# Optimization experiments

Hardware: AMD Instinct MI355X
Metric: run time of the kernel (lower is better)

Reference implementation:

```python
import jax, jax.numpy as jnp
import numpy as np

N_NODES = 100000
N_EDGES = 1600000
D_IN = 512
D_HID = 128
N_CLASSES = 100


def _gcn_norm(edge_index, n_nodes):
    # Add self loops and compute symmetric normalization D^{-1/2} (A+I) D^{-1/2}
    sl = jnp.arange(n_nodes, dtype=edge_index.dtype)
    src = jnp.concatenate([edge_index[0], sl])
    dst = jnp.concatenate([edge_index[1], sl])
    deg = jax.ops.segment_sum(jnp.ones_like(dst, dtype=jnp.float32), dst,
                              num_segments=n_nodes)
    dinv = jnp.where(deg > 0, jax.lax.rsqrt(deg), 0.0)
    norm = dinv[src] * dinv[dst]  # [E + N]
    return src, dst, norm


def _gcn_layer(x, W, b, src, dst, norm, n_nodes):
    h = x @ W                                  # [N, d_out] (transform first, like PyG GCNConv)
    msg = h[src] * norm[:, None]               # [E+N, d_out] gather + scale
    out = jax.ops.segment_sum(msg, dst, num_segments=n_nodes)  # scatter-add
    return out + b


def setup_inputs() -> dict:
    key = jax.random.key(0)
    ks = jax.random.split(key, 6)
    x = jax.random.normal(ks[0], (N_NODES, D_IN), dtype=jnp.float32)
    edge_index = jax.random.randint(ks[1], (2, N_EDGES), 0, N_NODES, dtype=jnp.int64)
    W1 = jax.random.normal(ks[2], (D_IN, D_HID), dtype=jnp.float32) * (1.0 / np.sqrt(D_IN))
    b1 = jnp.zeros((D_HID,), dtype=jnp.float32)
    W2 = jax.random.normal(ks[3], (D_HID, N_CLASSES), dtype=jnp.float32) * (1.0 / np.sqrt(D_HID))
    b2 = jnp.zeros((N_CLASSES,), dtype=jnp.float32)
    return {"x": x, "edge_index": edge_index, "W1": W1, "b1": b1, "W2": W2, "b2": b2}


def reference(x, edge_index, W1, b1, W2, b2):
    n_nodes = x.shape[0]
    src, dst, norm = _gcn_norm(edge_index, n_nodes)
    h = jax.nn.relu(_gcn_layer(x, W1, b1, src, dst, norm, n_nodes))
    logits = _gcn_layer(h, W2, b2, src, dst, norm, n_nodes)
    return jax.nn.log_softmax(logits, axis=-1)
```

## Files before the change

kernel.cpp:

```cpp
#include <hip/hip_runtime.h>
#include <math.h>

typedef __attribute__((ext_vector_type(8))) short short8;
typedef __attribute__((ext_vector_type(4))) float f32x4;
typedef _Float16 half8 __attribute__((ext_vector_type(8)));
typedef __fp16 fp16x2 __attribute__((ext_vector_type(2)));
typedef unsigned int uint;

__device__ inline uint f2bf(float f) {
    uint u = __float_as_uint(f);
    return (u + 0x7fffu + ((u >> 16) & 1u)) >> 16;
}
__device__ inline uint pack2(float lo, float hi) { return f2bf(lo) | (f2bf(hi) << 16); }
__device__ inline float bflo(uint u) { return __uint_as_float(u << 16); }
__device__ inline float bfhi(uint u) { return __uint_as_float(u & 0xffff0000u); }
__device__ inline uint cvtpk(float lo, float hi) {
    uint r;
    asm("v_cvt_pk_bf16_f32 %0, %1, %2" : "=v"(r) : "v"(lo), "v"(hi));
    return r;
}
__device__ inline uint pkh(float lo, float hi) {
    union { fp16x2 h; uint u; } c;
    c.h = __builtin_amdgcn_cvt_pkrtz(lo, hi);
    return c.u;
}

__global__ void k_degree(const int* __restrict__ dst, int E, int* __restrict__ cnt) {
    int i = blockIdx.x * 256 + threadIdx.x;
    if (i < E) atomicAdd(&cnt[dst[i]], 1);
}

__global__ void k_dinv(const int* __restrict__ cnt, float* __restrict__ dinv, int N) {
    int i = blockIdx.x * 256 + threadIdx.x;
    if (i < N) dinv[i] = rsqrtf((float)(cnt[i] + 1));
}

__global__ __launch_bounds__(512) void k_scan1(const int* __restrict__ cnt, int* __restrict__ rp,
                                               int* __restrict__ partials, int N) {
    __shared__ int s[512];
    int i = blockIdx.x * 512 + threadIdx.x;
    int v = (i < N) ? cnt[i] : 0;
    s[threadIdx.x] = v;
    __syncthreads();
    for (int d = 1; d < 512; d <<= 1) {
        int t = (threadIdx.x >= d) ? s[threadIdx.x - d] : 0;
        __syncthreads();
        s[threadIdx.x] += t;
        __syncthreads();
    }
    if (i < N) rp[i] = s[threadIdx.x] - v;
    if (threadIdx.x == 511) partials[blockIdx.x] = s[511];
}

__global__ void k_scan2(int* __restrict__ partials, int nb) {
    if (threadIdx.x == 0 && blockIdx.x == 0) {
        int acc = 0;
        for (int i = 0; i < nb; i++) { int v = partials[i]; partials[i] = acc; acc += v; }
    }
}

__global__ __launch_bounds__(512) void k_scan3(int* __restrict__ rp, const int* __restrict__ partials,
                                               int N, int E) {
    int i = blockIdx.x * 512 + threadIdx.x;
    if (i < N) rp[i] += partials[blockIdx.x];
    if (i == 0) rp[N] = E;
}

__global__ void k_fill(const int* __restrict__ src, const int* __restrict__ dst, int E,
                       const int* __restrict__ rp, int* __restrict__ cursor,
                       const float* __restrict__ dinv, float2* __restrict__ colw) {
    int i = blockIdx.x * 256 + threadIdx.x;
    if (i < E) {
        int d = dst[i];
        int s = src[i];
        int pos = rp[d] + atomicAdd(&cursor[d], 1);
        colw[pos] = make_float2(__int_as_float(s), dinv[s]);
    }
}

__global__ void k_w1prep(const float* __restrict__ W1, ushort* __restrict__ frag) {
    int tid = blockIdx.x * 256 + threadIdx.x;
    if (tid < 8192) {
        int ks = tid >> 9;
        int t = (tid >> 6) & 7;
        int l = tid & 63;
        int kbase = ks * 32 + (l >> 4) * 8;
        int c = t * 16 + (l & 15);
#pragma unroll
        for (int j = 0; j < 8; j++) {
            float v = W1[(size_t)(kbase + j) * 128 + c];
            union { _Float16 h; ushort u; } cv;
            cv.h = (_Float16)v;
            frag[(size_t)tid * 8 + j] = cv.u;
        }
    }
}

__global__ __launch_bounds__(256) void k_gemm1(const float* __restrict__ x,
                                               const uint4* __restrict__ w1f,
                                               uint* __restrict__ h1, int N) {
    __shared__ uint hsp[4][32][66];
    int tid = threadIdx.x, wv = tid >> 6, l = tid & 63;
    int cl = l & 15, kg = l >> 4;
    int n0 = blockIdx.x * 128 + wv * 32;
    int r0 = n0 + cl;       if (r0 >= N) r0 = N - 1;
    int r1 = n0 + 16 + cl;  if (r1 >= N) r1 = N - 1;
    const float* xr0 = x + (size_t)r0 * 512 + kg * 8;
    const float* xr1 = x + (size_t)r1 * 512 + kg * 8;

    f32x4 acc[2][8];
#pragma unroll
    for (int m = 0; m < 2; m++)
#pragma unroll
        for (int t = 0; t < 8; t++) acc[m][t] = (f32x4){0.f, 0.f, 0.f, 0.f};

    union U { uint4 u4; half8 h8; };

    float4 pa0[2], pa1[2];
    pa0[0] = *(const float4*)(xr0);     pa1[0] = *(const float4*)(xr0 + 4);
    pa0[1] = *(const float4*)(xr1);     pa1[1] = *(const float4*)(xr1 + 4);

    for (int ks = 0; ks < 16; ks++) {
        U A[2];
#pragma unroll
        for (int m = 0; m < 2; m++) {
            A[m].u4.x = pkh(pa0[m].x, pa0[m].y);
            A[m].u4.y = pkh(pa0[m].z, pa0[m].w);
            A[m].u4.z = pkh(pa1[m].x, pa1[m].y);
            A[m].u4.w = pkh(pa1[m].z, pa1[m].w);
        }
        uint4 bq[8];
#pragma unroll
        for (int t = 0; t < 8; t++) bq[t] = w1f[(ks * 8 + t) * 64 + l];
        if (ks < 15) {
            pa0[0] = *(const float4*)(xr0 + (ks + 1) * 32);
            pa1[0] = *(const float4*)(xr0 + (ks + 1) * 32 + 4);
            pa0[1] = *(const float4*)(xr1 + (ks + 1) * 32);
            pa1[1] = *(const float4*)(xr1 + (ks + 1) * 32 + 4);
        }
#pragma unroll
        for (int t = 0; t < 8; t++) {
            U B;
            B.u4 = bq[t];
            acc[0][t] = __builtin_amdgcn_mfma_f32_16x16x32_f16(A[0].h8, B.h8, acc[0][t], 0, 0, 0);
            acc[1][t] = __builtin_amdgcn_mfma_f32_16x16x32_f16(A[1].h8, B.h8, acc[1][t], 0, 0, 0);
        }
    }

#pragma unroll
    for (int m = 0; m < 2; m++)
#pragma unroll
        for (int t = 0; t < 8; t++)
#pragma unroll
            for (int r = 0; r < 4; r++) {
                float mine = acc[m][t][r];
                float other = __shfl_xor(mine, 1, 64);
                if ((cl & 1) == 0)
                    hsp[wv][m * 16 + kg * 4 + r][t * 8 + (cl >> 1)] = cvtpk(mine, other);
            }
#pragma unroll
    for (int it = 0; it < 32; it++) {
        int gr = n0 + it;
        if (gr < N) h1[(size_t)gr * 64 + l] = hsp[wv][it][l];
    }
}

template <bool RELU_BIAS>
__global__ __launch_bounds__(256) void k_agg(const uint* __restrict__ h, const float* __restrict__ dinv,
                                             const int* __restrict__ rp, const float2* __restrict__ colw,
                                             const float* __restrict__ bias, uint* __restrict__ outb, int N) {
    int wave = threadIdx.x >> 6, lane = threadIdx.x & 63;
    int v = blockIdx.x * 4 + wave;
    if (v >= N) return;
    float dv = dinv[v];
    float wself = dv * dv;
    uint us = h[(size_t)v * 64 + lane];
    float acc0 = bflo(us) * wself;
    float acc1 = bfhi(us) * wself;
    int e0 = rp[v], e1 = rp[v + 1];
    int i = e0;
    for (; i + 8 <= e1; i += 8) {
        float2 q[8];
        uint u[8];
#pragma unroll
        for (int j = 0; j < 8; j++) q[j] = colw[i + j];
#pragma unroll
        for (int j = 0; j < 8; j++) u[j] = h[(size_t)__float_as_int(q[j].x) * 64 + lane];
#pragma unroll
        for (int j = 0; j < 8; j++) {
            float w = q[j].y * dv;
            acc0 = fmaf(bflo(u[j]), w, acc0);
            acc1 = fmaf(bfhi(u[j]), w, acc1);
        }
    }
    if (i + 4 <= e1) {
        float2 q[4];
        uint u[4];
#pragma unroll
        for (int j = 0; j < 4; j++) q[j] = colw[i + j];
#pragma unroll
        for (int j = 0; j < 4; j++) u[j] = h[(size_t)__float_as_int(q[j].x) * 64 + lane];
#pragma unroll
        for (int j = 0; j < 4; j++) {
            float w = q[j].y * dv;
            acc0 = fmaf(bflo(u[j]), w, acc0);
            acc1 = fmaf(bfhi(u[j]), w, acc1);
        }
        i += 4;
    }
    for (; i < e1; i++) {
        float2 q = colw[i];
        uint u = h[(size_t)__float_as_int(q.x) * 64 + lane];
        float w = q.y * dv;
        acc0 = fmaf(bflo(u), w, acc0);
        acc1 = fmaf(bfhi(u), w, acc1);
    }
    if (RELU_BIAS) {
        float2 b = *(const float2*)&bias[2 * lane];
        acc0 = fmaxf(acc0 + b.x, 0.f);
        acc1 = fmaxf(acc1 + b.y, 0.f);
    }
    outb[(size_t)v * 64 + lane] = pack2(acc0, acc1);
}

__global__ void k_w2prep(const float* __restrict__ W2, const float* __restrict__ b2,
                         ushort* __restrict__ frag, float* __restrict__ b2pad) {
    int tid = blockIdx.x * 256 + threadIdx.x;
    if (tid < 1792) {
        int q = tid / 448;
        int t = (tid >> 6) % 7;
        int l = tid & 63;
        int kbase = q * 32 + (l >> 4) * 8;
        int c = t * 16 + (l & 15);
#pragma unroll
        for (int j = 0; j < 8; j++) {
            float v = (c < 100) ? W2[(kbase + j) * 100 + c] : 0.f;
            frag[(size_t)tid * 8 + j] = (ushort)f2bf(v);
        }
    } else if (tid < 1792 + 112) {
        int c = tid - 1792;
        b2pad[c] = (c < 100) ? b2[c] : -1e30f;
    }
}

__global__ __launch_bounds__(256) void k_out_mfma(const uint* __restrict__ g2u,
                                                  const uint4* __restrict__ w2fragG,
                                                  const float* __restrict__ b2pad,
                                                  float* __restrict__ out, int N) {
    __shared__ uint4 w2s[1792];
    __shared__ float b2s[112];
    int tid = threadIdx.x;
    for (int i = tid; i < 1792; i += 256) w2s[i] = w2fragG[i];
    if (tid < 112) b2s[tid] = b2pad[tid];
    __syncthreads();

    int w = tid >> 6, l = tid & 63;
    int v0 = blockIdx.x * 128 + w * 32;
    int cl = l & 15, gq = l >> 4;

    f32x4 acc[2][7];
#pragma unroll
    for (int m = 0; m < 2; m++)
#pragma unroll
        for (int t = 0; t < 7; t++) acc[m][t] = (f32x4){0.f, 0.f, 0.f, 0.f};

    union U { uint4 u4; short8 s8; };

#pragma unroll
    for (int q = 0; q < 4; q++) {
        short8 afr[2];
#pragma unroll
        for (int m = 0; m < 2; m++) {
            int rv = v0 + m * 16 + cl;
            if (rv >= N) rv = N - 1;
            U a;
            a.u4 = *(const uint4*)&g2u[(size_t)rv * 64 + q * 16 + gq * 4];
            afr[m] = a.s8;
        }
#pragma unroll
        for (int t = 0; t < 7; t++) {
            U b;
            b.u4 = w2s[(q * 7 + t) * 64 + l];
            acc[0][t] = __builtin_amdgcn_mfma_f32_16x16x32_bf16(afr[0], b.s8, acc[0][t], 0, 0, 0);
            acc[1][t] = __builtin_amdgcn_mfma_f32_16x16x32_bf16(afr[1], b.s8, acc[1][t], 0, 0, 0);
        }
    }

    float bsv[7];
#pragma unroll
    for (int t = 0; t < 7; t++) bsv[t] = b2s[t * 16 + cl];

#pragma unroll
    for (int m = 0; m < 2; m++) {
#pragma unroll
        for (int r = 0; r < 4; r++) {
            int row = v0 + m * 16 + gq * 4 + r;
            float lg[7];
#pragma unroll
            for (int t = 0; t < 7; t++) lg[t] = acc[m][t][r] + bsv[t];
            float mx = lg[0];
#pragma unroll
            for (int t = 1; t < 7; t++) mx = fmaxf(mx, lg[t]);
            mx = fmaxf(mx, __shfl_xor(mx, 1, 64));
            mx = fmaxf(mx, __shfl_xor(mx, 2, 64));
            mx = fmaxf(mx, __shfl_xor(mx, 4, 64));
            mx = fmaxf(mx, __shfl_xor(mx, 8, 64));
            float s = 0.f;
#pragma unroll
            for (int t = 0; t < 7; t++) s += __expf(lg[t] - mx);
            s += __shfl_xor(s, 1, 64);
            s += __shfl_xor(s, 2, 64);
            s += __shfl_xor(s, 4, 64);
            s += __shfl_xor(s, 8, 64);
            float lse = mx + __logf(s);
            if (row < N) {
#pragma unroll
                for (int t = 0; t < 7; t++) {
                    int c = t * 16 + cl;
                    if (c < 100) out[(size_t)row * 100 + c] = lg[t] - lse;
                }
            }
        }
    }
}

extern "C" void kernel_launch(void* const* d_in, const int* in_sizes, int n_in,
                              void* d_out, int out_size, void* d_ws, size_t ws_size,
                              hipStream_t stream) {
    const float* x  = (const float*)d_in[0];
    const int*   ei = (const int*)d_in[1];
    const float* W1 = (const float*)d_in[2];
    const float* b1 = (const float*)d_in[3];
    const float* W2 = (const float*)d_in[4];
    const float* b2 = (const float*)d_in[5];
    float* out = (float*)d_out;

    int N = in_sizes[0] / 512;
    int E = in_sizes[1] / 2;
    const int* srcI = ei;
    const int* dstI = ei + E;

    char* wsb = (char*)d_ws;
    size_t off = 0;
    auto alloc = [&](size_t bytes) {
        void* p = wsb + off;
        off = (off + bytes + 255) & ~(size_t)255;
        return p;
    };
    int*    cnt      = (int*)alloc((size_t)N * 4);
    int*    cursor   = (int*)alloc((size_t)N * 4);
    float*  dinv     = (float*)alloc((size_t)N * 4);
    int*    rp       = (int*)alloc((size_t)(N + 1) * 4);
    int*    partials = (int*)alloc(1024 * 4);
    ushort* w1f      = (ushort*)alloc(8192 * 8 * 2);
    ushort* w2frag   = (ushort*)alloc(1792 * 8 * 2);
    float*  b2pad    = (float*)alloc(112 * 4);
    float2* colw     = (float2*)alloc((size_t)E * 8);
    uint*   h1       = (uint*)alloc((size_t)N * 64 * 4);
    uint*   a1       = (uint*)alloc((size_t)N * 64 * 4);
    uint*   g2       = h1;

    hipMemsetAsync(cnt, 0, (size_t)N * 4, stream);
    hipMemsetAsync(cursor, 0, (size_t)N * 4, stream);

    k_degree<<<(E + 255) / 256, 256, 0, stream>>>(dstI, E, cnt);
    k_dinv<<<(N + 255) / 256, 256, 0, stream>>>(cnt, dinv, N);
    int nb = (N + 511) / 512;
    k_scan1<<<nb, 512, 0, stream>>>(cnt, rp, partials, N);
    k_scan2<<<1, 64, 0, stream>>>(partials, nb);
    k_scan3<<<nb, 512, 0, stream>>>(rp, partials, N, E);
    k_fill<<<(E + 255) / 256, 256, 0, stream>>>(srcI, dstI, E, rp, cursor, dinv, colw);
    k_w1prep<<<32, 256, 0, stream>>>(W1, w1f);
    k_w2prep<<<8, 256, 0, stream>>>(W2, b2, w2frag, b2pad);

    k_gemm1<<<(N + 127) / 128, 256, 0, stream>>>(x, (const uint4*)w1f, h1, N);
    k_agg<true><<<(N + 3) / 4, 256, 0, stream>>>(h1, dinv, rp, colw, b1, a1, N);
    k_agg<false><<<(N + 3) / 4, 256, 0, stream>>>(a1, dinv, rp, colw, nullptr, g2, N);
    k_out_mfma<<<(N + 127) / 128, 256, 0, stream>>>(g2, (const uint4*)w2frag, b2pad, out, N);
}
```

Before: 428.6 us.

## Stage GEMM1 x and W1 tiles through LDS with async double-buffered loads

Rewrites the first-layer GEMM so each block of 64 rows stages x and W1 fragment chunks into a 128KB double-buffered LDS region using global_load_lds, with an XOR swizzle on the x rows. Previously each wave streamed x and W1 straight from global memory into registers. The goal is to overlap the next chunk's loads with MFMA work and to share W1 across waves. In exchange, 128KB of LDS limits occupancy to one block per CU, and the tile shrinks from 128 to 64 rows per block.

```diff
diff --git a/kernel.cpp b/kernel.cpp
--- a/kernel.cpp
+++ b/kernel.cpp
@@ -23,6 +23,11 @@
     union { fp16x2 h; uint u; } c;
     c.h = __builtin_amdgcn_cvt_pkrtz(lo, hi);
     return c.u;
+}
+__device__ inline void gload16(const void* g, void* l) {
+    __builtin_amdgcn_global_load_lds(
+        (const __attribute__((address_space(1))) void*)g,
+        (__attribute__((address_space(3))) void*)l, 16, 0, 0);
 }
 
 __global__ void k_degree(const int* __restrict__ dst, int E, int* __restrict__ cnt) {
@@ -99,69 +104,75 @@
 __global__ __launch_bounds__(256) void k_gemm1(const float* __restrict__ x,
                                                const uint4* __restrict__ w1f,
                                                uint* __restrict__ h1, int N) {
-    __shared__ uint hsp[4][32][66];
+    __shared__ char lds[131072];
     int tid = threadIdx.x, wv = tid >> 6, l = tid & 63;
     int cl = l & 15, kg = l >> 4;
-    int n0 = blockIdx.x * 128 + wv * 32;
-    int r0 = n0 + cl;       if (r0 >= N) r0 = N - 1;
-    int r1 = n0 + 16 + cl;  if (r1 >= N) r1 = N - 1;
-    const float* xr0 = x + (size_t)r0 * 512 + kg * 8;
-    const float* xr1 = x + (size_t)r1 * 512 + kg * 8;
-
-    f32x4 acc[2][8];
-#pragma unroll
-    for (int m = 0; m < 2; m++)
-#pragma unroll
-        for (int t = 0; t < 8; t++) acc[m][t] = (f32x4){0.f, 0.f, 0.f, 0.f};
+    int row0 = blockIdx.x * 64;
+
+    auto stage = [&](int c) {
+        char* xbase = lds + (c & 1) * 32768;
+        char* bbase = lds + 65536 + (c & 1) * 32768;
+        const char* bsrc = (const char*)w1f + (size_t)(c * 2048) * 16;
+#pragma unroll
+        for (int i = 0; i < 8; i++) {
+            int s = wv * 512 + i * 64 + l;
+            int row = s >> 5, kk = s & 31;
+            int kslot = kk ^ (row & 7);
+            int rg = row0 + row; if (rg >= N) rg = N - 1;
+            const float* gs = x + (size_t)rg * 512 + c * 128 + kslot * 4;
+            gload16(gs, xbase + (size_t)(s - l) * 16);
+            gload16(bsrc + (size_t)s * 16, bbase + (size_t)(s - l) * 16);
+        }
+    };
+
+    f32x4 acc[8];
+#pragma unroll
+    for (int t = 0; t < 8; t++) acc[t] = (f32x4){0.f, 0.f, 0.f, 0.f};
 
     union U { uint4 u4; half8 h8; };
-
-    float4 pa0[2], pa1[2];
-    pa0[0] = *(const float4*)(xr0);     pa1[0] = *(const float4*)(xr0 + 4);
-    pa0[1] = *(const float4*)(xr1);     pa1[1] = *(const float4*)(xr1 + 4);
-
-    for (int ks = 0; ks < 16; ks++) {
-        U A[2];
-#pragma unroll
-        for (int m = 0; m < 2; m++) {
-            A[m].u4.x = pkh(pa0[m].x, pa0[m].y);
-            A[m].u4.y = pkh(pa0[m].z, pa0[m].w);
-            A[m].u4.z = pkh(pa1[m].x, pa1[m].y);
-            A[m].u4.w = pkh(pa1[m].z, pa1[m].w);
-        }
-        uint4 bq[8];
-#pragma unroll
-        for (int t = 0; t < 8; t++) bq[t] = w1f[(ks * 8 + t) * 64 + l];
-        if (ks < 15) {
-            pa0[0] = *(const float4*)(xr0 + (ks + 1) * 32);
-            pa1[0] = *(const float4*)(xr0 + (ks + 1) * 32 + 4);
-            pa0[1] = *(const float4*)(xr1 + (ks + 1) * 32);
-            pa1[1] = *(const float4*)(xr1 + (ks + 1) * 32 + 4);
-        }
-#pragma unroll
-        for (int t = 0; t < 8; t++) {
-            U B;
-            B.u4 = bq[t];
-            acc[0][t] = __builtin_amdgcn_mfma_f32_16x16x32_f16(A[0].h8, B.h8, acc[0][t], 0, 0, 0);
-            acc[1][t] = __builtin_amdgcn_mfma_f32_16x16x32_f16(A[1].h8, B.h8, acc[1][t], 0, 0, 0);
-        }
-    }
-
-#pragma unroll
-    for (int m = 0; m < 2; m++)
-#pragma unroll
-        for (int t = 0; t < 8; t++)
-#pragma unroll
-            for (int r = 0; r < 4; r++) {
-                float mine = acc[m][t][r];
-                float other = __shfl_xor(mine, 1, 64);
-                if ((cl & 1) == 0)
-                    hsp[wv][m * 16 + kg * 4 + r][t * 8 + (cl >> 1)] = cvtpk(mine, other);
+    int rowl = wv * 16 + cl;
+    int swz = cl & 7;
+
+    stage(0);
+    __syncthreads();
+    for (int c = 0; c < 4; c++) {
+        if (c < 3) stage(c + 1);
+        const char* xbase = lds + (c & 1) * 32768;
+        const char* bbase = lds + 65536 + (c & 1) * 32768;
+#pragma unroll
+        for (int ks = 0; ks < 4; ks++) {
+            int k4 = ks * 8 + kg * 2;
+            float4 a0 = *(const float4*)(xbase + (size_t)(rowl * 32 + (k4 ^ swz)) * 16);
+            float4 a1 = *(const float4*)(xbase + (size_t)(rowl * 32 + ((k4 + 1) ^ swz)) * 16);
+            U A;
+            A.u4.x = pkh(a0.x, a0.y);
+            A.u4.y = pkh(a0.z, a0.w);
+            A.u4.z = pkh(a1.x, a1.y);
+            A.u4.w = pkh(a1.z, a1.w);
+#pragma unroll
+            for (int t = 0; t < 8; t++) {
+                U B;
+                B.u4 = *(const uint4*)(bbase + (size_t)(((ks * 8 + t) * 64 + l)) * 16);
+                acc[t] = __builtin_amdgcn_mfma_f32_16x16x32_f16(A.h8, B.h8, acc[t], 0, 0, 0);
             }
-#pragma unroll
-    for (int it = 0; it < 32; it++) {
-        int gr = n0 + it;
-        if (gr < N) h1[(size_t)gr * 64 + l] = hsp[wv][it][l];
+        }
+        if (c < 3) __syncthreads();
+    }
+
+    uint* hsp = (uint*)lds;
+#pragma unroll
+    for (int t = 0; t < 8; t++)
+#pragma unroll
+        for (int r = 0; r < 4; r++) {
+            float mine = acc[t][r];
+            float other = __shfl_xor(mine, 1, 64);
+            if ((cl & 1) == 0)
+                hsp[(wv * 16 + kg * 4 + r) * 66 + t * 8 + (cl >> 1)] = cvtpk(mine, other);
+        }
+#pragma unroll
+    for (int it = 0; it < 16; it++) {
+        int gr = row0 + wv * 16 + it;
+        if (gr < N) h1[(size_t)gr * 64 + l] = hsp[(wv * 16 + it) * 66 + l];
     }
 }
 
@@ -373,7 +384,7 @@
     k_w1prep<<<32, 256, 0, stream>>>(W1, w1f);
     k_w2prep<<<8, 256, 0, stream>>>(W2, b2, w2frag, b2pad);
 
-    k_gemm1<<<(N + 127) / 128, 256, 0, stream>>>(x, (const uint4*)w1f, h1, N);
+    k_gemm1<<<(N + 63) / 64, 256, 0, stream>>>(x, (const uint4*)w1f, h1, N);
     k_agg<true><<<(N + 3) / 4, 256, 0, stream>>>(h1, dinv, rp, colw, b1, a1, N);
     k_agg<false><<<(N + 3) / 4, 256, 0, stream>>>(a1, dinv, rp, colw, nullptr, g2, N);
     k_out_mfma<<<(N + 127) / 128, 256, 0, stream>>>(g2, (const uint4*)w2frag, b2pad, out, N);
```

Measured after the change: 425.1 us. About the same (-0.8%).
